# Optimization experiments

Hardware: AMD Instinct MI355X
Metric: run time of the kernel (lower is better)

Reference implementation:

```python
import jax, jax.numpy as jnp
import numpy as np

H = 16        # num_heads
HD = 64       # head_dim = hidden_dim // num_heads
D = 1024      # hidden_dim
L = 1024      # seq_len (must be <= hidden_dim due to S_struc slicing)
B = 4         # batch
TOPK = 102    # int(0.1 * L)
SCALE = 8.0   # sqrt(head_dim)


def setup_inputs() -> dict:
    key = jax.random.key(0)
    ks = jax.random.split(key, 6)
    s = 0.02
    return {
        "x": jax.random.normal(ks[0], (L, B, D), jnp.float32),
        "qkv_w": jax.random.normal(ks[1], (3 * D, D), jnp.float32) * s,
        "qkv_b": jnp.zeros((3 * D,), jnp.float32),
        "out_w": jax.random.normal(ks[2], (D, D), jnp.float32) * s,
        "out_b": jnp.zeros((D,), jnp.float32),
        # S_struc is initialized positive in the original (ones/hidden_dim); keep it positive
        "S_struc": jax.random.uniform(ks[3], (H, D, D), jnp.float32, 1e-3, 1.0),
    }


def reference(x, qkv_w, qkv_b, out_w, out_b, S_struc):
    Ldim, Bdim, Dd = x.shape
    qkv = x @ qkv_w.T + qkv_b                      # (L,B,3D)
    q, k, v = jnp.split(qkv, 3, axis=-1)

    def to_hb(t):  # (L,B,D) -> (H,B,L,hd)
        return jnp.transpose(t.reshape(Ldim, Bdim, H, HD), (2, 1, 0, 3))

    q, k, v = to_hb(q), to_hb(k), to_hb(v)
    scores = jnp.einsum('hblf,hbtf->hblt', q, k) / SCALE          # (H,B,L,L)
    bias = jnp.log(S_struc[:, :Ldim, :Ldim] + 1e-8)[:, None]       # (H,1,L,L) per-head log-bias
    scores = scores + bias

    # data-dependent top-k sparse mask (scatter 0 at top-k positions, -inf elsewhere)
    idx = jax.lax.top_k(scores, TOPK)[1]                           # (H,B,L,k)
    h_i = jnp.arange(H)[:, None, None, None]
    b_i = jnp.arange(Bdim)[None, :, None, None]
    l_i = jnp.arange(Ldim)[None, None, :, None]
    mask = jnp.full(scores.shape, -jnp.inf, scores.dtype)
    mask = mask.at[h_i, b_i, l_i, idx].set(0.0)

    w = jax.nn.softmax(scores + mask, axis=-1)                     # (H,B,L,L)
    out = jnp.einsum('hblt,hbtv->hblv', w, v)                      # (H,B,L,hd)
    out = jnp.transpose(out, (2, 1, 0, 3)).reshape(Ldim, Bdim, Dd) # (L,B,D)
    return out @ out_w.T + out_b
```

## Files before the change

kernel.cpp:

```cpp
#include <hip/hip_runtime.h>
#include <math.h>

#define H 16
#define HD 64
#define DDIM 1024
#define LSEQ 1024
#define BATCH 4
#define TOPK 102
#define INV_SCALE 0.125f
#define MROWS (LSEQ * BATCH)
#define QKVN (3 * DDIM)
#define HBL (H * BATCH * LSEQ)
#define RPB 8

#define BM 128
#define BN 128
#define BKK 16

template <bool PERMUTE>
__global__ __launch_bounds__(256)
void gemm_abT_bias(const float* __restrict__ A, const float* __restrict__ Bw,
                   const float* __restrict__ bias, float* __restrict__ C,
                   int Nd, int Kd) {
    __shared__ float As[BKK][BM + 4];
    __shared__ float Bs[BKK][BN + 4];
    const int tid = threadIdx.x;
    const int tx = tid & 15, ty = tid >> 4;
    const int bn = blockIdx.x * BN, bm = blockIdx.y * BM;
    const int lr = tid >> 1;
    const int lc = (tid & 1) * 8;
    const float* Aptr = A + (size_t)(bm + lr) * Kd + lc;
    const float* Bptr = Bw + (size_t)(bn + lr) * Kd + lc;

    float acc[2][2][4][4];
    #pragma unroll
    for (int r = 0; r < 2; ++r)
        #pragma unroll
        for (int c = 0; c < 2; ++c)
            #pragma unroll
            for (int i = 0; i < 4; ++i)
                #pragma unroll
                for (int j = 0; j < 4; ++j) acc[r][c][i][j] = 0.0f;

    float4 av0 = *(const float4*)(Aptr);
    float4 av1 = *(const float4*)(Aptr + 4);
    float4 bv0 = *(const float4*)(Bptr);
    float4 bv1 = *(const float4*)(Bptr + 4);

    for (int k0 = 0; k0 < Kd; k0 += BKK) {
        __syncthreads();
        As[lc + 0][lr] = av0.x; As[lc + 1][lr] = av0.y; As[lc + 2][lr] = av0.z; As[lc + 3][lr] = av0.w;
        As[lc + 4][lr] = av1.x; As[lc + 5][lr] = av1.y; As[lc + 6][lr] = av1.z; As[lc + 7][lr] = av1.w;
        Bs[lc + 0][lr] = bv0.x; Bs[lc + 1][lr] = bv0.y; Bs[lc + 2][lr] = bv0.z; Bs[lc + 3][lr] = bv0.w;
        Bs[lc + 4][lr] = bv1.x; Bs[lc + 5][lr] = bv1.y; Bs[lc + 6][lr] = bv1.z; Bs[lc + 7][lr] = bv1.w;
        __syncthreads();
        if (k0 + BKK < Kd) {
            av0 = *(const float4*)(Aptr + k0 + BKK);
            av1 = *(const float4*)(Aptr + k0 + BKK + 4);
            bv0 = *(const float4*)(Bptr + k0 + BKK);
            bv1 = *(const float4*)(Bptr + k0 + BKK + 4);
        }
        #pragma unroll
        for (int kk = 0; kk < BKK; ++kk) {
            float ar[8], br[8];
            *(float4*)&ar[0] = *(const float4*)&As[kk][ty * 4];
            *(float4*)&ar[4] = *(const float4*)&As[kk][64 + ty * 4];
            *(float4*)&br[0] = *(const float4*)&Bs[kk][tx * 4];
            *(float4*)&br[4] = *(const float4*)&Bs[kk][64 + tx * 4];
            #pragma unroll
            for (int r = 0; r < 2; ++r)
                #pragma unroll
                for (int i = 0; i < 4; ++i)
                    #pragma unroll
                    for (int c = 0; c < 2; ++c)
                        #pragma unroll
                        for (int j = 0; j < 4; ++j)
                            acc[r][c][i][j] += ar[r * 4 + i] * br[c * 4 + j];
        }
    }
    float4 bb[2];
    bb[0] = *(const float4*)&bias[bn + tx * 4];
    bb[1] = *(const float4*)&bias[bn + 64 + tx * 4];
    #pragma unroll
    for (int r = 0; r < 2; ++r)
        #pragma unroll
        for (int i = 0; i < 4; ++i) {
            const int row = bm + r * 64 + ty * 4 + i;
            #pragma unroll
            for (int c = 0; c < 2; ++c) {
                float4 o;
                o.x = acc[r][c][i][0] + bb[c].x;
                o.y = acc[r][c][i][1] + bb[c].y;
                o.z = acc[r][c][i][2] + bb[c].z;
                o.w = acc[r][c][i][3] + bb[c].w;
                if (!PERMUTE) {
                    *(float4*)&C[(size_t)row * Nd + bn + c * 64 + tx * 4] = o;
                } else {
                    const int col = bn + c * 64 + tx * 4;
                    const int which = col >> 10;
                    const int hh = (col >> 6) & 15;
                    const int d = col & 63;
                    const int l = row >> 2, b2 = row & 3;
                    float* dst = C + (size_t)which * ((size_t)HBL * HD)
                               + (((size_t)(hh * BATCH + b2) * LSEQ + l) * HD + d);
                    *(float4*)dst = o;
                }
            }
        }
}

__global__ __launch_bounds__(512)
void fused_attn(const float* __restrict__ Q, const float* __restrict__ K,
                const float* __restrict__ V, const float* __restrict__ S,
                float* __restrict__ attn) {
    __shared__ unsigned sc[RPB][LSEQ];
    __shared__ int      hist[RPB][256];
    __shared__ float    qs[RPB][HD];
    __shared__ int      idxs[RPB][TOPK];
    __shared__ float    wts[RPB][TOPK];

    const int h = blockIdx.z, b = blockIdx.y, l0 = blockIdx.x * RPB;
    const int tid = threadIdx.x;
    const size_t hb = (size_t)(h * BATCH + b) * LSEQ;

    if (tid < 128) {
        const int r = tid >> 4, d4 = (tid & 15) * 4;
        *(float4*)&qs[r][d4] = *(const float4*)&Q[(hb + l0 + r) * HD + d4];
    }
    __syncthreads();

    #pragma unroll 1
    for (int j = 0; j < 2; ++j) {
        const int t = tid + j * 512;
        const float* kp = K + (hb + t) * HD;
        float ar[RPB];
        #pragma unroll
        for (int r = 0; r < RPB; ++r) ar[r] = 0.0f;
        #pragma unroll 8
        for (int dc = 0; dc < 16; ++dc) {
            const float4 kv = *(const float4*)(kp + dc * 4);
            #pragma unroll
            for (int r = 0; r < RPB; ++r) {
                const float4 q4 = *(const float4*)&qs[r][dc * 4];
                ar[r] += q4.x * kv.x + q4.y * kv.y + q4.z * kv.z + q4.w * kv.w;
            }
        }
        const float* Srow = S + (size_t)h * DDIM * DDIM + t;
        #pragma unroll
        for (int r = 0; r < RPB; ++r) {
            const float v = ar[r] * INV_SCALE + __logf(Srow[(size_t)(l0 + r) * DDIM] + 1e-8f);
            const unsigned bits = __float_as_uint(v);
            sc[r][t] = ((int)bits < 0) ? ~bits : (bits | 0x80000000u);
        }
    }
    __syncthreads();

    const int w = tid >> 6, lane = tid & 63;
    const unsigned long long lt = (1ull << lane) - 1ull;
    const unsigned* skey = sc[w];

    unsigned mxu = 0;
    #pragma unroll
    for (int i = 0; i < 16; ++i) {
        const unsigned k = skey[i * 64 + lane];
        mxu = (k > mxu) ? k : mxu;
    }
    #pragma unroll
    for (int off = 32; off; off >>= 1) {
        const unsigned o2 = (unsigned)__shfl_xor((int)mxu, off);
        mxu = (o2 > mxu) ? o2 : mxu;
    }
    const unsigned mbits = (mxu & 0x80000000u) ? (mxu & 0x7fffffffu) : ~mxu;
    const float mxf = __uint_as_float(mbits);

    unsigned prefix = 0, thr = 0;
    int need = TOPK;
    bool early = false;
    for (int pass = 0; pass < 4; ++pass) {
        const int shift = 24 - 8 * pass;
        hist[w][lane] = 0; hist[w][lane + 64] = 0;
        hist[w][lane + 128] = 0; hist[w][lane + 192] = 0;
        #pragma unroll
        for (int i = 0; i < 16; ++i) {
            const unsigned k = skey[i * 64 + lane];
            if (pass == 0 || (k >> (shift + 8)) == prefix) {
                const unsigned bkt = (k >> shift) & 255u;
                atomicAdd(&hist[w][(bkt & 3u) * 64 + (bkt >> 2)], 1);
            }
        }
        const int c0 = hist[w][lane];
        const int c1 = hist[w][64 + lane];
        const int c2 = hist[w][128 + lane];
        const int c3 = hist[w][192 + lane];
        int Ssum = c0 + c1 + c2 + c3;
        #pragma unroll
        for (int off = 1; off < 64; off <<= 1) {
            const int t2 = __shfl_down(Ssum, off);
            if (lane + off < 64) Ssum += t2;
        }
        const unsigned long long bal = __ballot(Ssum >= need);
        const int lstar = (int)__popcll(bal) - 1;
        const int above = (lstar < 63) ? __shfl(Ssum, lstar + 1) : 0;
        const int b0 = __shfl(c0, lstar), b1 = __shfl(c1, lstar);
        const int b2 = __shfl(c2, lstar), b3 = __shfl(c3, lstar);
        const int s3 = above + b3, s2 = s3 + b2, s1 = s2 + b1;
        int dstar, cbkt, selab;
        if (s3 >= need)      { dstar = 3; cbkt = b3; selab = above; }
        else if (s2 >= need) { dstar = 2; cbkt = b2; selab = s3; }
        else if (s1 >= need) { dstar = 1; cbkt = b1; selab = s2; }
        else                 { dstar = 0; cbkt = b0; selab = s1; }
        prefix = (prefix << 8) | (unsigned)(lstar * 4 + dstar);
        need -= selab;
        if (cbkt == need) { early = true; thr = prefix << shift; break; }
    }
    if (!early) thr = prefix;

    float lsum = 0.0f;
    int pos = 0, cum = 0;
    #pragma unroll
    for (int i = 0; i < 16; ++i) {
        const unsigned k = skey[i * 64 + lane];
        bool sel;
        if (early) {
            sel = (k >= thr);
        } else {
            const bool eq = (k == thr);
            const unsigned long long em = __ballot(eq);
            const int erank = cum + (int)__popcll(em & lt);
            cum += (int)__popcll(em);
            sel = (k > thr) || (eq && erank < need);
        }
        const unsigned long long sm = __ballot(sel);
        float pe = 0.0f;
        if (sel) {
            const unsigned bits = (k & 0x80000000u) ? (k & 0x7fffffffu) : ~k;
            pe = __expf(__uint_as_float(bits) - mxf);
            const int mypos = pos + (int)__popcll(sm & lt);
            idxs[w][mypos] = i * 64 + lane;
            wts[w][mypos] = pe;
        }
        pos += (int)__popcll(sm);
        lsum += pe;
    }
    #pragma unroll
    for (int off = 32; off; off >>= 1) lsum += __shfl_xor(lsum, off);
    const float inv = 1.0f / lsum;

    const float* vb = V + hb * HD + lane;
    float o0 = 0.0f, o1 = 0.0f;
    for (int j = 0; j < TOPK; j += 2) {
        const int2 ii = *(const int2*)&idxs[w][j];
        const float2 ww = *(const float2*)&wts[w][j];
        o0 += ww.x * vb[(size_t)ii.x * HD];
        o1 += ww.y * vb[(size_t)ii.y * HD];
    }
    attn[((size_t)(l0 + w) * BATCH + b) * DDIM + h * HD + lane] = (o0 + o1) * inv;
}

extern "C" void kernel_launch(void* const* d_in, const int* in_sizes, int n_in,
                              void* d_out, int out_size, void* d_ws, size_t ws_size,
                              hipStream_t stream) {
    (void)in_sizes; (void)n_in; (void)out_size; (void)ws_size;
    const float* x      = (const float*)d_in[0];
    const float* qkv_w  = (const float*)d_in[1];
    const float* qkv_b  = (const float*)d_in[2];
    const float* out_w  = (const float*)d_in[3];
    const float* out_b  = (const float*)d_in[4];
    const float* S      = (const float*)d_in[5];
    float* out = (float*)d_out;

    float* Q    = (float*)d_ws;
    float* Kb   = Q + (size_t)HBL * HD;
    float* V    = Kb + (size_t)HBL * HD;
    float* attn = V + (size_t)HBL * HD;

    gemm_abT_bias<true><<<dim3(QKVN / BN, MROWS / BM), 256, 0, stream>>>(
        x, qkv_w, qkv_b, Q, QKVN, DDIM);

    fused_attn<<<dim3(LSEQ / RPB, BATCH, H), 512, 0, stream>>>(Q, Kb, V, S, attn);

    gemm_abT_bias<false><<<dim3(DDIM / BN, MROWS / BM), 256, 0, stream>>>(
        attn, out_w, out_b, out, DDIM, DDIM);
}
```

Baseline: 1.070 ms.

## Replace FP32 SIMT GEMMs with split-bf16 MFMA GEMMs emulating fp32 precision

```diff
diff --git a/kernel.cpp b/kernel.cpp
--- a/kernel.cpp
+++ b/kernel.cpp
@@ -13,106 +13,192 @@
 #define HBL (H * BATCH * LSEQ)
 #define RPB 8
 
-#define BM 128
-#define BN 128
-#define BKK 16
+typedef __attribute__((ext_vector_type(8))) short bf16x8;
+typedef __attribute__((ext_vector_type(4))) float f32x4;
+
+__device__ __forceinline__ unsigned short f2bf(float f) {
+    unsigned u = __float_as_uint(f);
+    u += 0x7FFFu + ((u >> 16) & 1u);
+    return (unsigned short)(u >> 16);
+}
+__device__ __forceinline__ float bf2f(unsigned short h) {
+    return __uint_as_float(((unsigned)h) << 16);
+}
+
+__global__ __launch_bounds__(256)
+void split_bf16(const float* __restrict__ src, unsigned short* __restrict__ dh,
+                unsigned short* __restrict__ dl, int n4) {
+    for (int i = blockIdx.x * 256 + threadIdx.x; i < n4; i += gridDim.x * 256) {
+        const float4 v = ((const float4*)src)[i];
+        ushort4 h, l;
+        h.x = f2bf(v.x); l.x = f2bf(v.x - bf2f(h.x));
+        h.y = f2bf(v.y); l.y = f2bf(v.y - bf2f(h.y));
+        h.z = f2bf(v.z); l.z = f2bf(v.z - bf2f(h.z));
+        h.w = f2bf(v.w); l.w = f2bf(v.w - bf2f(h.w));
+        ((ushort4*)dh)[i] = h;
+        ((ushort4*)dl)[i] = l;
+    }
+}
+
+__global__ __launch_bounds__(256)
+void split3_bf16(const float* __restrict__ src, unsigned short* __restrict__ dh,
+                 unsigned short* __restrict__ dl, unsigned short* __restrict__ dm, int n4) {
+    for (int i = blockIdx.x * 256 + threadIdx.x; i < n4; i += gridDim.x * 256) {
+        const float4 v = ((const float4*)src)[i];
+        ushort4 h, l, m;
+        float r;
+        h.x = f2bf(v.x); r = v.x - bf2f(h.x); l.x = f2bf(r); m.x = f2bf(r - bf2f(l.x));
+        h.y = f2bf(v.y); r = v.y - bf2f(h.y); l.y = f2bf(r); m.y = f2bf(r - bf2f(l.y));
+        h.z = f2bf(v.z); r = v.z - bf2f(h.z); l.z = f2bf(r); m.z = f2bf(r - bf2f(l.z));
+        h.w = f2bf(v.w); r = v.w - bf2f(h.w); l.w = f2bf(r); m.w = f2bf(r - bf2f(l.w));
+        ((ushort4*)dh)[i] = h;
+        ((ushort4*)dl)[i] = l;
+        ((ushort4*)dm)[i] = m;
+    }
+}
 
 template <bool PERMUTE>
 __global__ __launch_bounds__(256)
-void gemm_abT_bias(const float* __restrict__ A, const float* __restrict__ Bw,
-                   const float* __restrict__ bias, float* __restrict__ C,
-                   int Nd, int Kd) {
-    __shared__ float As[BKK][BM + 4];
-    __shared__ float Bs[BKK][BN + 4];
+void gemm_bf16x3(const unsigned short* __restrict__ Ah, const unsigned short* __restrict__ Al,
+                 const unsigned short* __restrict__ Am,
+                 const unsigned short* __restrict__ Bh, const unsigned short* __restrict__ Bl,
+                 const unsigned short* __restrict__ Bm,
+                 const float* __restrict__ bias, float* __restrict__ C,
+                 int Nd, int Kd) {
     const int tid = threadIdx.x;
-    const int tx = tid & 15, ty = tid >> 4;
-    const int bn = blockIdx.x * BN, bm = blockIdx.y * BM;
-    const int lr = tid >> 1;
-    const int lc = (tid & 1) * 8;
-    const float* Aptr = A + (size_t)(bm + lr) * Kd + lc;
-    const float* Bptr = Bw + (size_t)(bn + lr) * Kd + lc;
-
-    float acc[2][2][4][4];
-    #pragma unroll
-    for (int r = 0; r < 2; ++r)
-        #pragma unroll
-        for (int c = 0; c < 2; ++c)
-            #pragma unroll
-            for (int i = 0; i < 4; ++i)
-                #pragma unroll
-                for (int j = 0; j < 4; ++j) acc[r][c][i][j] = 0.0f;
-
-    float4 av0 = *(const float4*)(Aptr);
-    float4 av1 = *(const float4*)(Aptr + 4);
-    float4 bv0 = *(const float4*)(Bptr);
-    float4 bv1 = *(const float4*)(Bptr + 4);
-
-    for (int k0 = 0; k0 < Kd; k0 += BKK) {
-        __syncthreads();
-        As[lc + 0][lr] = av0.x; As[lc + 1][lr] = av0.y; As[lc + 2][lr] = av0.z; As[lc + 3][lr] = av0.w;
-        As[lc + 4][lr] = av1.x; As[lc + 5][lr] = av1.y; As[lc + 6][lr] = av1.z; As[lc + 7][lr] = av1.w;
-        Bs[lc + 0][lr] = bv0.x; Bs[lc + 1][lr] = bv0.y; Bs[lc + 2][lr] = bv0.z; Bs[lc + 3][lr] = bv0.w;
-        Bs[lc + 4][lr] = bv1.x; Bs[lc + 5][lr] = bv1.y; Bs[lc + 6][lr] = bv1.z; Bs[lc + 7][lr] = bv1.w;
-        __syncthreads();
-        if (k0 + BKK < Kd) {
-            av0 = *(const float4*)(Aptr + k0 + BKK);
-            av1 = *(const float4*)(Aptr + k0 + BKK + 4);
-            bv0 = *(const float4*)(Bptr + k0 + BKK);
-            bv1 = *(const float4*)(Bptr + k0 + BKK + 4);
-        }
-        #pragma unroll
-        for (int kk = 0; kk < BKK; ++kk) {
-            float ar[8], br[8];
-            *(float4*)&ar[0] = *(const float4*)&As[kk][ty * 4];
-            *(float4*)&ar[4] = *(const float4*)&As[kk][64 + ty * 4];
-            *(float4*)&br[0] = *(const float4*)&Bs[kk][tx * 4];
-            *(float4*)&br[4] = *(const float4*)&Bs[kk][64 + tx * 4];
-            #pragma unroll
-            for (int r = 0; r < 2; ++r)
-                #pragma unroll
-                for (int i = 0; i < 4; ++i)
-                    #pragma unroll
-                    for (int c = 0; c < 2; ++c)
-                        #pragma unroll
-                        for (int j = 0; j < 4; ++j)
-                            acc[r][c][i][j] += ar[r * 4 + i] * br[c * 4 + j];
-        }
-    }
-    float4 bb[2];
-    bb[0] = *(const float4*)&bias[bn + tx * 4];
-    bb[1] = *(const float4*)&bias[bn + 64 + tx * 4];
-    #pragma unroll
-    for (int r = 0; r < 2; ++r)
+    const int w = tid >> 6, lane = tid & 63;
+    const int bmt = blockIdx.y * 128, bnt = blockIdx.x * 128;
+    const int wm = (w >> 1) * 64, wn = (w & 1) * 64;
+    const int r16 = lane & 15, ch = lane >> 4;
+
+    const size_t arow0 = (size_t)(bmt + wm + r16);
+    const size_t brow0 = (size_t)(bnt + wn + r16);
+
+    f32x4 acc[4][4] = {};
+
+    for (int k0 = 0; k0 < Kd; k0 += 32) {
+        const size_t koff = (size_t)k0 + ch * 8;
+        bf16x8 ah[4], al[4], am[4];
         #pragma unroll
         for (int i = 0; i < 4; ++i) {
-            const int row = bm + r * 64 + ty * 4 + i;
-            #pragma unroll
-            for (int c = 0; c < 2; ++c) {
-                float4 o;
-                o.x = acc[r][c][i][0] + bb[c].x;
-                o.y = acc[r][c][i][1] + bb[c].y;
-                o.z = acc[r][c][i][2] + bb[c].z;
-                o.w = acc[r][c][i][3] + bb[c].w;
+            const size_t ao = (arow0 + i * 16) * Kd + koff;
+            ah[i] = *(const bf16x8*)(Ah + ao);
+            al[i] = *(const bf16x8*)(Al + ao);
+            am[i] = *(const bf16x8*)(Am + ao);
+        }
+        #pragma unroll
+        for (int j = 0; j < 4; ++j) {
+            const size_t bo = (brow0 + j * 16) * Kd + koff;
+            const bf16x8 bh = *(const bf16x8*)(Bh + bo);
+            const bf16x8 bl = *(const bf16x8*)(Bl + bo);
+            const bf16x8 bm8 = *(const bf16x8*)(Bm + bo);
+            #pragma unroll
+            for (int i = 0; i < 4; ++i) {
+                acc[i][j] = __builtin_amdgcn_mfma_f32_16x16x32_bf16(ah[i], bh, acc[i][j], 0, 0, 0);
+                acc[i][j] = __builtin_amdgcn_mfma_f32_16x16x32_bf16(ah[i], bl, acc[i][j], 0, 0, 0);
+                acc[i][j] = __builtin_amdgcn_mfma_f32_16x16x32_bf16(al[i], bh, acc[i][j], 0, 0, 0);
+                acc[i][j] = __builtin_amdgcn_mfma_f32_16x16x32_bf16(al[i], bl, acc[i][j], 0, 0, 0);
+                acc[i][j] = __builtin_amdgcn_mfma_f32_16x16x32_bf16(ah[i], bm8, acc[i][j], 0, 0, 0);
+                acc[i][j] = __builtin_amdgcn_mfma_f32_16x16x32_bf16(am[i], bh, acc[i][j], 0, 0, 0);
+            }
+        }
+    }
+
+    float bj[4];
+    #pragma unroll
+    for (int j = 0; j < 4; ++j) bj[j] = bias[bnt + wn + j * 16 + r16];
+
+    #pragma unroll
+    for (int i = 0; i < 4; ++i) {
+        #pragma unroll
+        for (int r = 0; r < 4; ++r) {
+            const int R = bmt + wm + i * 16 + ch * 4 + r;
+            #pragma unroll
+            for (int j = 0; j < 4; ++j) {
+                const float v = acc[i][j][r] + bj[j];
+                const int Cc = bnt + wn + j * 16 + r16;
                 if (!PERMUTE) {
-                    *(float4*)&C[(size_t)row * Nd + bn + c * 64 + tx * 4] = o;
+                    C[(size_t)R * Nd + Cc] = v;
                 } else {
-                    const int col = bn + c * 64 + tx * 4;
-                    const int which = col >> 10;
-                    const int hh = (col >> 6) & 15;
-                    const int d = col & 63;
-                    const int l = row >> 2, b2 = row & 3;
-                    float* dst = C + (size_t)which * ((size_t)HBL * HD)
-                               + (((size_t)(hh * BATCH + b2) * LSEQ + l) * HD + d);
-                    *(float4*)dst = o;
+                    const int which = Cc >> 10, hh = (Cc >> 6) & 15, d = Cc & 63;
+                    const int l = R >> 2, b2 = R & 3;
+                    C[(size_t)which * ((size_t)HBL * HD)
+                      + (((size_t)(hh * BATCH + b2) * LSEQ + l) * HD + d)] = v;
                 }
             }
         }
+    }
+}
+
+template <bool PERMUTE>
+__global__ __launch_bounds__(256)
+void gemm_bf16x2(const unsigned short* __restrict__ Ah, const unsigned short* __restrict__ Al,
+                 const unsigned short* __restrict__ Bh, const unsigned short* __restrict__ Bl,
+                 const float* __restrict__ bias, float* __restrict__ C,
+                 int Nd, int Kd) {
+    const int tid = threadIdx.x;
+    const int w = tid >> 6, lane = tid & 63;
+    const int bmt = blockIdx.y * 128, bnt = blockIdx.x * 128;
+    const int wm = (w >> 1) * 64, wn = (w & 1) * 64;
+    const int r16 = lane & 15, ch = lane >> 4;
+
+    const size_t arow0 = (size_t)(bmt + wm + r16);
+    const size_t brow0 = (size_t)(bnt + wn + r16);
+
+    f32x4 acc[4][4] = {};
+
+    for (int k0 = 0; k0 < Kd; k0 += 32) {
+        const size_t koff = (size_t)k0 + ch * 8;
+        bf16x8 ah[4], al[4], bh[4], bl[4];
+        #pragma unroll
+        for (int i = 0; i < 4; ++i) {
+            const size_t ao = (arow0 + i * 16) * Kd + koff;
+            ah[i] = *(const bf16x8*)(Ah + ao);
+            al[i] = *(const bf16x8*)(Al + ao);
+            const size_t bo = (brow0 + i * 16) * Kd + koff;
+            bh[i] = *(const bf16x8*)(Bh + bo);
+            bl[i] = *(const bf16x8*)(Bl + bo);
+        }
+        #pragma unroll
+        for (int i = 0; i < 4; ++i)
+            #pragma unroll
+            for (int j = 0; j < 4; ++j) {
+                acc[i][j] = __builtin_amdgcn_mfma_f32_16x16x32_bf16(ah[i], bh[j], acc[i][j], 0, 0, 0);
+                acc[i][j] = __builtin_amdgcn_mfma_f32_16x16x32_bf16(ah[i], bl[j], acc[i][j], 0, 0, 0);
+                acc[i][j] = __builtin_amdgcn_mfma_f32_16x16x32_bf16(al[i], bh[j], acc[i][j], 0, 0, 0);
+            }
+    }
+
+    float bj[4];
+    #pragma unroll
+    for (int j = 0; j < 4; ++j) bj[j] = bias[bnt + wn + j * 16 + r16];
+
+    #pragma unroll
+    for (int i = 0; i < 4; ++i) {
+        #pragma unroll
+        for (int r = 0; r < 4; ++r) {
+            const int R = bmt + wm + i * 16 + ch * 4 + r;
+            #pragma unroll
+            for (int j = 0; j < 4; ++j) {
+                const float v = acc[i][j][r] + bj[j];
+                const int Cc = bnt + wn + j * 16 + r16;
+                if (!PERMUTE) {
+                    C[(size_t)R * Nd + Cc] = v;
+                } else {
+                    const int which = Cc >> 10, hh = (Cc >> 6) & 15, d = Cc & 63;
+                    const int l = R >> 2, b2 = R & 3;
+                    C[(size_t)which * ((size_t)HBL * HD)
+                      + (((size_t)(hh * BATCH + b2) * LSEQ + l) * HD + d)] = v;
+                }
+            }
+        }
+    }
 }
 
 __global__ __launch_bounds__(512)
 void fused_attn(const float* __restrict__ Q, const float* __restrict__ K,
                 const float* __restrict__ V, const float* __restrict__ S,
-                float* __restrict__ attn) {
+                unsigned short* __restrict__ attn_h, unsigned short* __restrict__ attn_l) {
     __shared__ unsigned sc[RPB][LSEQ];
     __shared__ int      hist[RPB][256];
     __shared__ float    qs[RPB][HD];
@@ -254,7 +340,11 @@
         o0 += ww.x * vb[(size_t)ii.x * HD];
         o1 += ww.y * vb[(size_t)ii.y * HD];
     }
-    attn[((size_t)(l0 + w) * BATCH + b) * DDIM + h * HD + lane] = (o0 + o1) * inv;
+    const float o = (o0 + o1) * inv;
+    const size_t oidx = ((size_t)(l0 + w) * BATCH + b) * DDIM + h * HD + lane;
+    const unsigned short hbits = f2bf(o);
+    attn_h[oidx] = hbits;
+    attn_l[oidx] = f2bf(o - bf2f(hbits));
 }
 
 extern "C" void kernel_launch(void* const* d_in, const int* in_sizes, int n_in,
@@ -269,16 +359,31 @@
     const float* S      = (const float*)d_in[5];
     float* out = (float*)d_out;
 
-    float* Q    = (float*)d_ws;
-    float* Kb   = Q + (size_t)HBL * HD;
-    float* V    = Kb + (size_t)HBL * HD;
-    float* attn = V + (size_t)HBL * HD;
-
-    gemm_abT_bias<true><<<dim3(QKVN / BN, MROWS / BM), 256, 0, stream>>>(
-        x, qkv_w, qkv_b, Q, QKVN, DDIM);
-
-    fused_attn<<<dim3(LSEQ / RPB, BATCH, H), 512, 0, stream>>>(Q, Kb, V, S, attn);
-
-    gemm_abT_bias<false><<<dim3(DDIM / BN, MROWS / BM), 256, 0, stream>>>(
-        attn, out_w, out_b, out, DDIM, DDIM);
-}
+    char* base = (char*)d_ws;
+    float* Q  = (float*)base;
+    float* Kb = Q + (size_t)HBL * HD;
+    float* V  = Kb + (size_t)HBL * HD;
+    unsigned short* xh = (unsigned short*)(V + (size_t)HBL * HD);
+    unsigned short* xl = xh + (size_t)MROWS * DDIM;
+    unsigned short* xm = xl + (size_t)MROWS * DDIM;
+    unsigned short* wh = xm + (size_t)MROWS * DDIM;
+    unsigned short* wl = wh + (size_t)QKVN * DDIM;
+    unsigned short* wm = wl + (size_t)QKVN * DDIM;
+    unsigned short* attn_h = xh;
+    unsigned short* attn_l = xl;
+    unsigned short* oh = wh;
+    unsigned short* ol = wl;
+
+    split3_bf16<<<1024, 256, 0, stream>>>(x,     xh, xl, xm, MROWS * DDIM / 4);
+    split3_bf16<<<1024, 256, 0, stream>>>(qkv_w, wh, wl, wm, QKVN * DDIM / 4);
+
+    gemm_bf16x3<true><<<dim3(QKVN / 128, MROWS / 128), 256, 0, stream>>>(
+        xh, xl, xm, wh, wl, wm, qkv_b, Q, QKVN, DDIM);
+
+    split_bf16<<<512, 256, 0, stream>>>(out_w, oh, ol, DDIM * DDIM / 4);
+
+    fused_attn<<<dim3(LSEQ / RPB, BATCH, H), 512, 0, stream>>>(Q, Kb, V, S, attn_h, attn_l);
+
+    gemm_bf16x2<false><<<dim3(DDIM / 128, MROWS / 128), 256, 0, stream>>>(
+        attn_h, attn_l, oh, ol, out_b, out, DDIM, DDIM);
+}
```

After: 1.003 ms. 6.2% less time.
